# Kernel tuning notes

Hardware: AMD Instinct MI355X
Metric: run time of the kernel (lower is better)

The kernel has to match this reference:

```python
import jax, jax.numpy as jnp
import numpy as np
from jax import lax

TAU_SYN = 0.5
TAU_MEM_MIN, TAU_MEM_MAX = 0.8, 0.98
VTH_MIN, VTH_MAX = 0.05, 0.5
ALPHA = 4.0  # surrogate sharpness (forward output unaffected)

B, T, N = 32, 128, 4096


def setup_inputs() -> dict:
    key = jax.random.key(0)
    k1, k2, k3 = jax.random.split(key, 3)
    x = jax.random.normal(k1, (B, T, N), dtype=jnp.float32)
    # learnable per-neuron decay / threshold, initialized inside their clamp ranges
    tau_mem = TAU_MEM_MIN + (TAU_MEM_MAX - TAU_MEM_MIN) * jax.random.uniform(k2, (N,), dtype=jnp.float32)
    v_threshold = VTH_MIN + (VTH_MAX - VTH_MIN) * jax.random.uniform(k3, (N,), dtype=jnp.float32)
    return {"x": x, "tau_mem": tau_mem, "v_threshold": v_threshold}


def _lin_scan(a, b):
    """Parallel scan of y[t] = a[t]*y[t-1] + b[t] along axis 1 (y[-1]=0)."""
    def combine(c1, c2):
        a1, b1 = c1
        a2, b2 = c2
        return a1 * a2, a2 * b1 + b2
    _, y = lax.associative_scan(combine, (a, b), axis=1)
    return y


def reference(x, tau_mem, v_threshold):
    tau_m = jnp.clip(tau_mem, TAU_MEM_MIN, TAU_MEM_MAX)          # (N,)
    thr = jnp.clip(v_threshold, VTH_MIN, VTH_MAX)                # (N,)
    # synaptic current: i_syn[t] = tau_syn * i_syn[t-1] + x[t]
    a_syn = jnp.full_like(x, TAU_SYN)
    i_syn = _lin_scan(a_syn, x)                                  # (B,T,N)
    # membrane: v[t] = tau_mem * v[t-1] + (1 - tau_mem) * i_syn[t]
    a_mem = jnp.broadcast_to(tau_m, x.shape)
    v_mem = _lin_scan(a_mem, (1.0 - tau_m) * i_syn)              # (B,T,N)
    # hard binary spikes (Heaviside at per-neuron threshold)
    spikes = (v_mem >= thr).astype(x.dtype)                      # (B,T,N)
    return spikes
```

## Files before the change

### kernel.cpp

```cpp
#include <hip/hip_runtime.h>

constexpr int B = 32;
constexpr int T = 128;
constexpr int N = 4096;
constexpr int UNR = 8;
constexpr int NG = T / UNR;

__global__ __launch_bounds__(256) void lif_scan_kernel(
    const float* __restrict__ x,
    const float* __restrict__ tau_mem,
    const float* __restrict__ v_th,
    float* __restrict__ out)
{
    const int tid = blockIdx.x * blockDim.x + threadIdx.x;
    const int b   = tid >> 12;
    const int n   = tid & (N - 1);

    const float tmf = fminf(fmaxf(tau_mem[n], 0.8f), 0.98f);
    const float thf = fminf(fmaxf(v_th[n],  0.05f), 0.5f);

    const double tm = (double)tmf;
    const double cm = 1.0 - tm;
    const double th = (double)thf;

    const size_t base = (size_t)b * T * N + (size_t)n;
    const float* xp = x + base;
    float*       op = out + base;

    double is = 0.0, v = 0.0;

    float buf[UNR];
#pragma unroll
    for (int u = 0; u < UNR; ++u)
        buf[u] = __builtin_nontemporal_load(xp + (size_t)u * N);

    for (int g = 0; g < NG; ++g) {
        float nbuf[UNR];
        if (g + 1 < NG) {
            const float* xg = xp + (size_t)(g + 1) * UNR * N;
#pragma unroll
            for (int u = 0; u < UNR; ++u)
                nbuf[u] = __builtin_nontemporal_load(xg + (size_t)u * N);
        }

        float* og = op + (size_t)g * UNR * N;
#pragma unroll
        for (int u = 0; u < UNR; ++u) {
            is = fma(0.5, is, (double)buf[u]);
            v = fma(tm, v, cm * is);
            __builtin_nontemporal_store((v >= th) ? 1.0f : 0.0f,
                                        og + (size_t)u * N);
        }

#pragma unroll
        for (int u = 0; u < UNR; ++u) buf[u] = nbuf[u];
    }
}

extern "C" void kernel_launch(void* const* d_in, const int* in_sizes, int n_in,
                              void* d_out, int out_size, void* d_ws, size_t ws_size,
                              hipStream_t stream) {
    const float* x       = (const float*)d_in[0];
    const float* tau_mem = (const float*)d_in[1];
    const float* v_th    = (const float*)d_in[2];
    float* out           = (float*)d_out;

    const int threads = B * N;
    dim3 block(256);
    dim3 grid(threads / 256);
    lif_scan_kernel<<<grid, block, 0, stream>>>(x, tau_mem, v_th, out);
}
```

Before: 124.3 us.

## Process two neurons per thread with float2 loads/stores and deeper prefetch

After: 111.5 us. -10.3%, faster.

```diff
diff --git a/kernel.cpp b/kernel.cpp
--- a/kernel.cpp
+++ b/kernel.cpp
@@ -3,8 +3,10 @@
 constexpr int B = 32;
 constexpr int T = 128;
 constexpr int N = 4096;
-constexpr int UNR = 8;
-constexpr int NG = T / UNR;
+constexpr int UNR = 16;
+constexpr int NG  = T / UNR;
+
+typedef float f32x2 __attribute__((ext_vector_type(2)));
 
 __global__ __launch_bounds__(256) void lif_scan_kernel(
     const float* __restrict__ x,
@@ -13,43 +15,49 @@
     float* __restrict__ out)
 {
     const int tid = blockIdx.x * blockDim.x + threadIdx.x;
-    const int b   = tid >> 12;
-    const int n   = tid & (N - 1);
+    const int b   = tid >> 11;
+    const int n2  = (tid & 2047) * 2;
 
-    const float tmf = fminf(fmaxf(tau_mem[n], 0.8f), 0.98f);
-    const float thf = fminf(fmaxf(v_th[n],  0.05f), 0.5f);
+    const f32x2 tm = *reinterpret_cast<const f32x2*>(tau_mem + n2);
+    const f32x2 tv = *reinterpret_cast<const f32x2*>(v_th + n2);
 
-    const double tm = (double)tmf;
-    const double cm = 1.0 - tm;
-    const double th = (double)thf;
+    const double t0 = (double)fminf(fmaxf(tm.x, 0.8f), 0.98f);
+    const double t1 = (double)fminf(fmaxf(tm.y, 0.8f), 0.98f);
+    const double c0 = 1.0 - t0, c1 = 1.0 - t1;
+    const double h0 = (double)fminf(fmaxf(tv.x, 0.05f), 0.5f);
+    const double h1 = (double)fminf(fmaxf(tv.y, 0.05f), 0.5f);
 
-    const size_t base = (size_t)b * T * N + (size_t)n;
+    const size_t base = (size_t)b * T * N + (size_t)n2;
     const float* xp = x + base;
     float*       op = out + base;
 
-    double is = 0.0, v = 0.0;
+    double is0 = 0.0, is1 = 0.0, v0 = 0.0, v1 = 0.0;
 
-    float buf[UNR];
+    f32x2 buf[UNR];
 #pragma unroll
     for (int u = 0; u < UNR; ++u)
-        buf[u] = __builtin_nontemporal_load(xp + (size_t)u * N);
+        buf[u] = *reinterpret_cast<const f32x2*>(xp + (size_t)u * N);
 
     for (int g = 0; g < NG; ++g) {
-        float nbuf[UNR];
+        f32x2 nbuf[UNR];
         if (g + 1 < NG) {
             const float* xg = xp + (size_t)(g + 1) * UNR * N;
 #pragma unroll
             for (int u = 0; u < UNR; ++u)
-                nbuf[u] = __builtin_nontemporal_load(xg + (size_t)u * N);
+                nbuf[u] = *reinterpret_cast<const f32x2*>(xg + (size_t)u * N);
         }
 
         float* og = op + (size_t)g * UNR * N;
 #pragma unroll
         for (int u = 0; u < UNR; ++u) {
-            is = fma(0.5, is, (double)buf[u]);
-            v = fma(tm, v, cm * is);
-            __builtin_nontemporal_store((v >= th) ? 1.0f : 0.0f,
-                                        og + (size_t)u * N);
+            is0 = fma(0.5, is0, (double)buf[u].x);
+            is1 = fma(0.5, is1, (double)buf[u].y);
+            v0 = fma(t0, v0, c0 * is0);
+            v1 = fma(t1, v1, c1 * is1);
+            f32x2 s;
+            s.x = (v0 >= h0) ? 1.0f : 0.0f;
+            s.y = (v1 >= h1) ? 1.0f : 0.0f;
+            __builtin_nontemporal_store(s, reinterpret_cast<f32x2*>(og + (size_t)u * N));
         }
 
 #pragma unroll
@@ -65,7 +73,7 @@
     const float* v_th    = (const float*)d_in[2];
     float* out           = (float*)d_out;
 
-    const int threads = B * N;
+    const int threads = B * (N / 2);
     dim3 block(256);
     dim3 grid(threads / 256);
     lif_scan_kernel<<<grid, block, 0, stream>>>(x, tau_mem, v_th, out);
```

## Vectorize LIF scan to four neurons per thread with 128-bit loads and stores

Applied to the files above, without the earlier changes.

New measurement: 116.5 us. -6.3%, faster.

```diff
diff --git a/kernel.cpp b/kernel.cpp
--- a/kernel.cpp
+++ b/kernel.cpp
@@ -4,52 +4,62 @@
 constexpr int T = 128;
 constexpr int N = 4096;
 constexpr int UNR = 8;
-constexpr int NG = T / UNR;
+constexpr int NG  = T / UNR;
 
-__global__ __launch_bounds__(256) void lif_scan_kernel(
+typedef float f32x4 __attribute__((ext_vector_type(4)));
+
+__global__ __launch_bounds__(128) void lif_scan_kernel(
     const float* __restrict__ x,
     const float* __restrict__ tau_mem,
     const float* __restrict__ v_th,
     float* __restrict__ out)
 {
     const int tid = blockIdx.x * blockDim.x + threadIdx.x;
-    const int b   = tid >> 12;
-    const int n   = tid & (N - 1);
+    const int b   = tid >> 10;
+    const int n4  = (tid & 1023) * 4;
 
-    const float tmf = fminf(fmaxf(tau_mem[n], 0.8f), 0.98f);
-    const float thf = fminf(fmaxf(v_th[n],  0.05f), 0.5f);
+    const f32x4 tm = *reinterpret_cast<const f32x4*>(tau_mem + n4);
+    const f32x4 tv = *reinterpret_cast<const f32x4*>(v_th + n4);
 
-    const double tm = (double)tmf;
-    const double cm = 1.0 - tm;
-    const double th = (double)thf;
+    double t[4], c[4], h[4], is[4], v[4];
+#pragma unroll
+    for (int k = 0; k < 4; ++k) {
+        t[k] = (double)fminf(fmaxf(tm[k], 0.8f), 0.98f);
+        c[k] = 1.0 - t[k];
+        h[k] = (double)fminf(fmaxf(tv[k], 0.05f), 0.5f);
+        is[k] = 0.0;
+        v[k]  = 0.0;
+    }
 
-    const size_t base = (size_t)b * T * N + (size_t)n;
+    const size_t base = (size_t)b * T * N + (size_t)n4;
     const float* xp = x + base;
     float*       op = out + base;
 
-    double is = 0.0, v = 0.0;
-
-    float buf[UNR];
+    f32x4 buf[UNR];
 #pragma unroll
     for (int u = 0; u < UNR; ++u)
-        buf[u] = __builtin_nontemporal_load(xp + (size_t)u * N);
+        buf[u] = *reinterpret_cast<const f32x4*>(xp + (size_t)u * N);
 
     for (int g = 0; g < NG; ++g) {
-        float nbuf[UNR];
+        f32x4 nbuf[UNR];
         if (g + 1 < NG) {
             const float* xg = xp + (size_t)(g + 1) * UNR * N;
 #pragma unroll
             for (int u = 0; u < UNR; ++u)
-                nbuf[u] = __builtin_nontemporal_load(xg + (size_t)u * N);
+                nbuf[u] = *reinterpret_cast<const f32x4*>(xg + (size_t)u * N);
         }
 
         float* og = op + (size_t)g * UNR * N;
 #pragma unroll
         for (int u = 0; u < UNR; ++u) {
-            is = fma(0.5, is, (double)buf[u]);
-            v = fma(tm, v, cm * is);
-            __builtin_nontemporal_store((v >= th) ? 1.0f : 0.0f,
-                                        og + (size_t)u * N);
+            f32x4 s;
+#pragma unroll
+            for (int k = 0; k < 4; ++k) {
+                is[k] = fma(0.5, is[k], (double)buf[u][k]);
+                v[k] = fma(t[k], v[k], c[k] * is[k]);
+                s[k] = (v[k] >= h[k]) ? 1.0f : 0.0f;
+            }
+            __builtin_nontemporal_store(s, reinterpret_cast<f32x4*>(og + (size_t)u * N));
         }
 
 #pragma unroll
@@ -65,8 +75,8 @@
     const float* v_th    = (const float*)d_in[2];
     float* out           = (float*)d_out;
 
-    const int threads = B * N;
-    dim3 block(256);
-    dim3 grid(threads / 256);
+    const int threads = B * (N / 4);
+    dim3 block(128);
+    dim3 grid(threads / 128);
     lif_scan_kernel<<<grid, block, 0, stream>>>(x, tau_mem, v_th, out);
 }
```
